# Optimization experiments

Hardware: AMD Instinct MI355X
Metric: run time of the kernel (lower is better)

The kernel has to match this reference:

```python
import jax, jax.numpy as jnp
import numpy as np

B, IN, OUT, K = 2048, 1024, 1024, 20


def setup_inputs() -> dict:
    key = jax.random.key(0)
    k1, k2 = jax.random.split(key)
    x = jax.random.normal(k1, (B, IN), dtype=jnp.float32)
    # per-output, per-input spline coefficients: (out_features, in_features, num_knots)
    W = jax.random.normal(k2, (OUT, IN, K), dtype=jnp.float32) * 0.1
    # evenly spaced knot grid on [-2, 2] (linspace)
    knots = jnp.linspace(-2.0, 2.0, K, dtype=jnp.float32)
    return {"x": x, "W": W, "knots": knots}


def reference(x, W, knots):
    # RBF spline basis shared across all output features (this is the fusion
    # the original per-output Python loop misses):
    # basis[b, i, k] = exp(-0.5 * ((x[b, i] - knots[k]) / h)^2)
    h = knots[1] - knots[0]  # uniform knot spacing -> RBF bandwidth
    basis = jnp.exp(-0.5 * jnp.square((x[:, :, None] - knots) / h))  # (B, IN, K)
    # Each SplineLayer o computes sum_{i,k} W[o,i,k] * basis[b,i,k]; the
    # KANBlock concatenates the OUT scalars -> a single einsum.
    return jnp.einsum("bik,oik->bo", basis, W)  # (B, OUT)
```

## Files before the change

### kernel.cpp

```cpp
#include <hip/hip_runtime.h>

#define B_DIM 2048
#define IN_DIM 1024
#define OUT_DIM 1024
#define K_KNOTS 20
#define KR (IN_DIM * K_KNOTS)
#define OUT_ELEMS (B_DIM * OUT_DIM)
#define KS 8

#define NPAIRS (B_DIM * IN_DIM * 5 / 2)
#define NB_BASIS_BLK (NPAIRS / 256)
#define NW4 (OUT_DIM * KR / 8)
#define NB_W_BLK (NW4 / 256)

typedef __bf16 bf16x8 __attribute__((ext_vector_type(8)));
typedef float  f32x4  __attribute__((ext_vector_type(4)));

#define MFMA16(a, b, c) __builtin_amdgcn_mfma_f32_16x16x32_bf16(a, b, c, 0, 0, 0)

__device__ __forceinline__ unsigned short f2bf(float f) {
    unsigned int u = __float_as_uint(f);
    unsigned int r = u + 0x7fffu + ((u >> 16) & 1u);
    return (unsigned short)(r >> 16);
}

__device__ __forceinline__ unsigned int pack2(float lo, float hi) {
    return (unsigned int)f2bf(lo) | ((unsigned int)f2bf(hi) << 16);
}

__device__ __forceinline__ void async_load16(const void* g, void* l) {
    __builtin_amdgcn_global_load_lds(
        (const __attribute__((address_space(1))) void*)g,
        (__attribute__((address_space(3))) void*)l,
        16, 0, 0);
}

__global__ void __launch_bounds__(256) prep_kernel(
        const float* __restrict__ x,
        const float4* __restrict__ Wsrc,
        const float* __restrict__ knots,
        uint4* __restrict__ basis_out,
        uint4* __restrict__ w_out) {
    if (blockIdx.x < NB_BASIS_BLK) {
        const unsigned int p  = blockIdx.x * 256 + threadIdx.x;
        const unsigned int n0 = 2 * p;
        const unsigned int q0  = n0 % 5u;
        const unsigned int bi0 = n0 / 5u;
        const float t0   = knots[0];
        const float h    = knots[1] - t0;
        const float invh = 1.0f / h;

        const bool cross = (q0 == 4u);
        const unsigned int bi1 = bi0 + (cross ? 1u : 0u);
        const float xv0 = x[bi0];
        const float xv1 = x[bi1];
        const float kA = (float)(4u * q0);
        const float kB = cross ? 0.f : kA + 4.f;

        float v[8];
#pragma unroll
        for (int j = 0; j < 4; ++j) {
            float t = __builtin_fmaf(kA + (float)j, h, t0);
            float d = (xv0 - t) * invh;
            v[j] = __expf(-0.5f * d * d);
        }
#pragma unroll
        for (int j = 0; j < 4; ++j) {
            float t = __builtin_fmaf(kB + (float)j, h, t0);
            float d = (xv1 - t) * invh;
            v[4 + j] = __expf(-0.5f * d * d);
        }
        uint4 o;
        o.x = pack2(v[0], v[1]); o.y = pack2(v[2], v[3]);
        o.z = pack2(v[4], v[5]); o.w = pack2(v[6], v[7]);
        basis_out[p] = o;
    } else {
        unsigned int t = (blockIdx.x - NB_BASIS_BLK) * 256 + threadIdx.x;
        float4 a = Wsrc[2 * t];
        float4 b = Wsrc[2 * t + 1];
        uint4 o;
        o.x = pack2(a.x, a.y);
        o.y = pack2(a.z, a.w);
        o.z = pack2(b.x, b.y);
        o.w = pack2(b.z, b.w);
        w_out[t] = o;
    }
}

#define AOF(s, kh) (((s) * 2 + (kh)) * 8192)
#define BOF(s, kh) (32768 + ((s) * 2 + (kh)) * 8192)

template <int S>
__device__ __forceinline__ void tile_step(
        int t, int ntiles,
        const unsigned short* __restrict__ Ab,
        const unsigned short* __restrict__ Bb,
        unsigned short* lds,
        f32x4 (&acc)[8][4],
        int m0, int n0, int k0,
        int wave, int rowA, int rowB,
        int srow32, int scol32) {
    const int kb1 = k0 + (t + 1) * 64;
    const bool st = (t + 1 < ntiles);

    auto stage_half = [&](const unsigned short* __restrict__ src, int grow,
                          int kc, int lbase) {
        const unsigned short* g =
            src + (size_t)(grow + wave * 32 + srow32) * KR + kc + scol32;
        async_load16(g,                   &lds[lbase + wave * 1024]);
        async_load16(g + (size_t)16 * KR, &lds[lbase + wave * 1024 + 512]);
    };

    bf16x8 a0[4], a1[4], b0[4], b1[4], s0[4], s1[4];

#pragma unroll
    for (int i = 0; i < 4; ++i) a0[i] = *(const bf16x8*)&lds[AOF(S, 0) + rowA + i * 512];
#pragma unroll
    for (int j = 0; j < 4; ++j) b0[j] = *(const bf16x8*)&lds[BOF(S, 0) + rowB + j * 512];
    if (st) {
        stage_half(Ab, m0, kb1, AOF(S ^ 1, 0));
        asm volatile("s_waitcnt vmcnt(2)" ::: "memory");
    } else {
        asm volatile("s_waitcnt vmcnt(0)" ::: "memory");
    }
    __builtin_amdgcn_s_barrier();
    asm volatile("s_waitcnt lgkmcnt(0)" ::: "memory");
    __builtin_amdgcn_sched_barrier(0);
    __builtin_amdgcn_s_setprio(1);
#pragma unroll
    for (int i = 0; i < 4; ++i)
#pragma unroll
        for (int j = 0; j < 4; ++j)
            acc[i][j] = MFMA16(a0[i], b0[j], acc[i][j]);
    __builtin_amdgcn_s_setprio(0);

#pragma unroll
    for (int i = 0; i < 4; ++i) a1[i] = *(const bf16x8*)&lds[AOF(S, 1) + rowA + i * 512];
#pragma unroll
    for (int j = 0; j < 4; ++j) b1[j] = *(const bf16x8*)&lds[BOF(S, 1) + rowB + j * 512];
    if (st) stage_half(Bb, n0, kb1, BOF(S ^ 1, 0));
    __builtin_amdgcn_s_barrier();
    asm volatile("s_waitcnt lgkmcnt(0)" ::: "memory");
    __builtin_amdgcn_sched_barrier(0);
    __builtin_amdgcn_s_setprio(1);
#pragma unroll
    for (int i = 0; i < 4; ++i)
#pragma unroll
        for (int j = 0; j < 4; ++j)
            acc[i][j] = MFMA16(a1[i], b1[j], acc[i][j]);
    __builtin_amdgcn_s_setprio(0);

#pragma unroll
    for (int i = 0; i < 4; ++i) s0[i] = *(const bf16x8*)&lds[AOF(S, 0) + rowA + (4 + i) * 512];
    if (st) stage_half(Ab, m0, kb1 + 32, AOF(S ^ 1, 1));
    __builtin_amdgcn_s_barrier();
    asm volatile("s_waitcnt lgkmcnt(0)" ::: "memory");
    __builtin_amdgcn_sched_barrier(0);
    __builtin_amdgcn_s_setprio(1);
#pragma unroll
    for (int i = 0; i < 4; ++i)
#pragma unroll
        for (int j = 0; j < 4; ++j)
            acc[4 + i][j] = MFMA16(s0[i], b0[j], acc[4 + i][j]);
    __builtin_amdgcn_s_setprio(0);

#pragma unroll
    for (int i = 0; i < 4; ++i) s1[i] = *(const bf16x8*)&lds[AOF(S, 1) + rowA + (4 + i) * 512];
    if (st) {
        stage_half(Bb, n0, kb1 + 32, BOF(S ^ 1, 1));
        asm volatile("s_waitcnt vmcnt(4)" ::: "memory");
    }
    __builtin_amdgcn_s_barrier();
    asm volatile("s_waitcnt lgkmcnt(0)" ::: "memory");
    __builtin_amdgcn_sched_barrier(0);
    __builtin_amdgcn_s_setprio(1);
#pragma unroll
    for (int i = 0; i < 4; ++i)
#pragma unroll
        for (int j = 0; j < 4; ++j)
            acc[4 + i][j] = MFMA16(s1[i], b1[j], acc[4 + i][j]);
    __builtin_amdgcn_s_setprio(0);
}

__global__ void __launch_bounds__(512, 2)
kan_gemm8(const unsigned short* __restrict__ Ab,
          const unsigned short* __restrict__ Bb,
          float* __restrict__ part) {
    __shared__ __align__(16) unsigned short lds[65536];

    constexpr int KPBk   = KR / KS;
    constexpr int NTILES = KPBk / 64;

    const int id  = blockIdx.x;
    const int z   = id & 7;
    const int ord = id >> 3;
    const int mt  = ord & 7;
    const int nt  = ord >> 3;
    const int m0  = mt * 256;
    const int n0  = nt * 256;
    const int k0  = z * KPBk;

    const int tid  = threadIdx.x;
    const int wave = tid >> 6;
    const int lane = tid & 63;
    const int wm   = wave >> 2;
    const int wn   = wave & 3;

    const int srow32 = lane >> 2;
    const int scol32 = ((lane & 3) ^ ((lane >> 3) & 3)) * 8;

    auto stage_half = [&](const unsigned short* __restrict__ src, int grow,
                          int kc, int lbase) {
        const unsigned short* g =
            src + (size_t)(grow + wave * 32 + srow32) * KR + kc + scol32;
        async_load16(g,                   &lds[lbase + wave * 1024]);
        async_load16(g + (size_t)16 * KR, &lds[lbase + wave * 1024 + 512]);
    };

    f32x4 acc[8][4];
#pragma unroll
    for (int i = 0; i < 8; ++i)
#pragma unroll
        for (int j = 0; j < 4; ++j) acc[i][j] = (f32x4){0.f, 0.f, 0.f, 0.f};

    const int q    = lane >> 4;
    const int r15  = lane & 15;
    const int cs   = (q ^ ((r15 >> 1) & 3)) * 8;
    const int rowA = (wm * 128 + r15) * 32 + cs;
    const int rowB = (wn * 64 + r15) * 32 + cs;

    stage_half(Ab, m0, k0,      AOF(0, 0));
    stage_half(Bb, n0, k0,      BOF(0, 0));
    stage_half(Ab, m0, k0 + 32, AOF(0, 1));
    stage_half(Bb, n0, k0 + 32, BOF(0, 1));
    asm volatile("s_waitcnt vmcnt(4)" ::: "memory");
    __builtin_amdgcn_s_barrier();

    for (int tt = 0; tt < NTILES; tt += 2) {
        tile_step<0>(tt,     NTILES, Ab, Bb, lds, acc, m0, n0, k0,
                     wave, rowA, rowB, srow32, scol32);
        tile_step<1>(tt + 1, NTILES, Ab, Bb, lds, acc, m0, n0, k0,
                     wave, rowA, rowB, srow32, scol32);
    }

    float* dst = part + (size_t)z * OUT_ELEMS;
#pragma unroll
    for (int i = 0; i < 8; ++i)
#pragma unroll
        for (int j = 0; j < 4; ++j)
#pragma unroll
            for (int r = 0; r < 4; ++r) {
                const int row = m0 + wm * 128 + i * 16 + q * 4 + r;
                const int c   = n0 + wn * 64  + j * 16 + r15;
                dst[(size_t)row * OUT_DIM + c] = acc[i][j][r];
            }
}

template <int KSr>
__global__ void kan_reduce(const float* __restrict__ part, float* __restrict__ out) {
    const int idx = (blockIdx.x * 256 + threadIdx.x) * 4;
    f32x4 s = *(const f32x4*)(part + idx);
#pragma unroll
    for (int z = 1; z < KSr; ++z)
        s += *(const f32x4*)(part + (size_t)z * OUT_ELEMS + idx);
    *(f32x4*)(out + idx) = s;
}

__global__ void kan_fallback(const float* __restrict__ x,
                             const float* __restrict__ W,
                             const float* __restrict__ knots,
                             float* __restrict__ out) {
    __shared__ float basis[256 * K_KNOTS];
    const int b = blockIdx.x;
    const int o = blockIdx.y * blockDim.x + threadIdx.x;
    const float invh = 1.0f / (knots[1] - knots[0]);
    const float* w = W + (size_t)o * KR;
    float sum = 0.f;
    for (int i0 = 0; i0 < IN_DIM; i0 += 256) {
        __syncthreads();
        for (int idx = threadIdx.x; idx < 256 * K_KNOTS; idx += blockDim.x) {
            const int i = i0 + idx / K_KNOTS;
            const int k = idx % K_KNOTS;
            const float d = (x[(size_t)b * IN_DIM + i] - knots[k]) * invh;
            basis[idx] = __expf(-0.5f * d * d);
        }
        __syncthreads();
        for (int r = 0; r < 256 * K_KNOTS; ++r)
            sum += basis[r] * w[(size_t)i0 * K_KNOTS + r];
    }
    out[(size_t)b * OUT_DIM + o] = sum;
}

extern "C" void kernel_launch(void* const* d_in, const int* in_sizes, int n_in,
                              void* d_out, int out_size, void* d_ws, size_t ws_size,
                              hipStream_t stream) {
    const float* x     = (const float*)d_in[0];
    const float* W     = (const float*)d_in[1];
    const float* knots = (const float*)d_in[2];
    float* out = (float*)d_out;

    const size_t basis_bytes = (size_t)B_DIM * KR * 2;
    const size_t wb_bytes    = (size_t)OUT_DIM * KR * 2;
    const size_t part_bytes  = (size_t)KS * OUT_ELEMS * 4;

    unsigned short* Ab = (unsigned short*)d_ws;
    unsigned short* Bb = (unsigned short*)((char*)d_ws + basis_bytes);
    float* part = (float*)((char*)d_ws + basis_bytes + wb_bytes);

    if (ws_size >= basis_bytes + wb_bytes + part_bytes) {
        prep_kernel<<<dim3(NB_BASIS_BLK + NB_W_BLK), dim3(256), 0, stream>>>(
            x, (const float4*)W, knots, (uint4*)Ab, (uint4*)Bb);
        kan_gemm8<<<dim3(256), dim3(512), 0, stream>>>(Ab, Bb, part);
        kan_reduce<KS><<<dim3(OUT_ELEMS / (256 * 4)), dim3(256), 0, stream>>>(part, out);
    } else {
        kan_fallback<<<dim3(B_DIM, OUT_DIM / 256), dim3(256), 0, stream>>>(x, W, knots, out);
    }
}
```

Baseline: 244.9 us.

## Prefetch next MFMA phase LDS fragments before current phase compute

Software-pipelines the LDS-to-register fragment loads in the GEMM tile step. Each phase now issues the reads for the next phase before running its MFMAs, and waits only with a partial lgkmcnt. The a0/b0 fragments of the next tile are loaded at the end of the previous tile and carried across calls. This aims to hide LDS read latency behind matrix-core work, at the cost of more live VGPRs and tighter reliance on the barrier ordering staying correct.

```diff
diff --git a/kernel.cpp b/kernel.cpp
--- a/kernel.cpp
+++ b/kernel.cpp
@@ -97,6 +97,7 @@
         const unsigned short* __restrict__ Bb,
         unsigned short* lds,
         f32x4 (&acc)[8][4],
+        bf16x8 (&a0)[4], bf16x8 (&b0)[4],
         int m0, int n0, int k0,
         int wave, int rowA, int rowB,
         int srow32, int scol32) {
@@ -111,12 +112,8 @@
         async_load16(g + (size_t)16 * KR, &lds[lbase + wave * 1024 + 512]);
     };
 
-    bf16x8 a0[4], a1[4], b0[4], b1[4], s0[4], s1[4];
-
-#pragma unroll
-    for (int i = 0; i < 4; ++i) a0[i] = *(const bf16x8*)&lds[AOF(S, 0) + rowA + i * 512];
-#pragma unroll
-    for (int j = 0; j < 4; ++j) b0[j] = *(const bf16x8*)&lds[BOF(S, 0) + rowB + j * 512];
+    bf16x8 a1[4], b1[4], s0[4], s1[4];
+
     if (st) {
         stage_half(Ab, m0, kb1, AOF(S ^ 1, 0));
         asm volatile("s_waitcnt vmcnt(2)" ::: "memory");
@@ -124,7 +121,13 @@
         asm volatile("s_waitcnt vmcnt(0)" ::: "memory");
     }
     __builtin_amdgcn_s_barrier();
-    asm volatile("s_waitcnt lgkmcnt(0)" ::: "memory");
+    asm volatile("" ::: "memory");
+#pragma unroll
+    for (int i = 0; i < 4; ++i) a1[i] = *(const bf16x8*)&lds[AOF(S, 1) + rowA + i * 512];
+#pragma unroll
+    for (int j = 0; j < 4; ++j) b1[j] = *(const bf16x8*)&lds[BOF(S, 1) + rowB + j * 512];
+    __builtin_amdgcn_sched_barrier(0);
+    asm volatile("s_waitcnt lgkmcnt(8)" ::: "memory");
     __builtin_amdgcn_sched_barrier(0);
     __builtin_amdgcn_s_setprio(1);
 #pragma unroll
@@ -134,13 +137,13 @@
             acc[i][j] = MFMA16(a0[i], b0[j], acc[i][j]);
     __builtin_amdgcn_s_setprio(0);
 
-#pragma unroll
-    for (int i = 0; i < 4; ++i) a1[i] = *(const bf16x8*)&lds[AOF(S, 1) + rowA + i * 512];
-#pragma unroll
-    for (int j = 0; j < 4; ++j) b1[j] = *(const bf16x8*)&lds[BOF(S, 1) + rowB + j * 512];
     if (st) stage_half(Bb, n0, kb1, BOF(S ^ 1, 0));
     __builtin_amdgcn_s_barrier();
-    asm volatile("s_waitcnt lgkmcnt(0)" ::: "memory");
+    asm volatile("" ::: "memory");
+#pragma unroll
+    for (int i = 0; i < 4; ++i) s0[i] = *(const bf16x8*)&lds[AOF(S, 0) + rowA + (4 + i) * 512];
+    __builtin_amdgcn_sched_barrier(0);
+    asm volatile("s_waitcnt lgkmcnt(4)" ::: "memory");
     __builtin_amdgcn_sched_barrier(0);
     __builtin_amdgcn_s_setprio(1);
 #pragma unroll
@@ -150,11 +153,13 @@
             acc[i][j] = MFMA16(a1[i], b1[j], acc[i][j]);
     __builtin_amdgcn_s_setprio(0);
 
-#pragma unroll
-    for (int i = 0; i < 4; ++i) s0[i] = *(const bf16x8*)&lds[AOF(S, 0) + rowA + (4 + i) * 512];
     if (st) stage_half(Ab, m0, kb1 + 32, AOF(S ^ 1, 1));
     __builtin_amdgcn_s_barrier();
-    asm volatile("s_waitcnt lgkmcnt(0)" ::: "memory");
+    asm volatile("" ::: "memory");
+#pragma unroll
+    for (int i = 0; i < 4; ++i) s1[i] = *(const bf16x8*)&lds[AOF(S, 1) + rowA + (4 + i) * 512];
+    __builtin_amdgcn_sched_barrier(0);
+    asm volatile("s_waitcnt lgkmcnt(4)" ::: "memory");
     __builtin_amdgcn_sched_barrier(0);
     __builtin_amdgcn_s_setprio(1);
 #pragma unroll
@@ -164,14 +169,22 @@
             acc[4 + i][j] = MFMA16(s0[i], b0[j], acc[4 + i][j]);
     __builtin_amdgcn_s_setprio(0);
 
-#pragma unroll
-    for (int i = 0; i < 4; ++i) s1[i] = *(const bf16x8*)&lds[AOF(S, 1) + rowA + (4 + i) * 512];
     if (st) {
         stage_half(Bb, n0, kb1 + 32, BOF(S ^ 1, 1));
         asm volatile("s_waitcnt vmcnt(4)" ::: "memory");
     }
     __builtin_amdgcn_s_barrier();
-    asm volatile("s_waitcnt lgkmcnt(0)" ::: "memory");
+    asm volatile("" ::: "memory");
+    if (st) {
+#pragma unroll
+        for (int i = 0; i < 4; ++i) a0[i] = *(const bf16x8*)&lds[AOF(S ^ 1, 0) + rowA + i * 512];
+#pragma unroll
+        for (int j = 0; j < 4; ++j) b0[j] = *(const bf16x8*)&lds[BOF(S ^ 1, 0) + rowB + j * 512];
+        __builtin_amdgcn_sched_barrier(0);
+        asm volatile("s_waitcnt lgkmcnt(8)" ::: "memory");
+    } else {
+        asm volatile("s_waitcnt lgkmcnt(0)" ::: "memory");
+    }
     __builtin_amdgcn_sched_barrier(0);
     __builtin_amdgcn_s_setprio(1);
 #pragma unroll
@@ -235,11 +248,18 @@
     stage_half(Bb, n0, k0 + 32, BOF(0, 1));
     asm volatile("s_waitcnt vmcnt(4)" ::: "memory");
     __builtin_amdgcn_s_barrier();
+    asm volatile("" ::: "memory");
+    bf16x8 a0[4], b0[4];
+#pragma unroll
+    for (int i = 0; i < 4; ++i) a0[i] = *(const bf16x8*)&lds[AOF(0, 0) + rowA + i * 512];
+#pragma unroll
+    for (int j = 0; j < 4; ++j) b0[j] = *(const bf16x8*)&lds[BOF(0, 0) + rowB + j * 512];
+    __builtin_amdgcn_sched_barrier(0);
 
     for (int tt = 0; tt < NTILES; tt += 2) {
-        tile_step<0>(tt,     NTILES, Ab, Bb, lds, acc, m0, n0, k0,
+        tile_step<0>(tt,     NTILES, Ab, Bb, lds, acc, a0, b0, m0, n0, k0,
                      wave, rowA, rowB, srow32, scol32);
-        tile_step<1>(tt + 1, NTILES, Ab, Bb, lds, acc, m0, n0, k0,
+        tile_step<1>(tt + 1, NTILES, Ab, Bb, lds, acc, a0, b0, m0, n0, k0,
                      wave, rowA, rowB, srow32, scol32);
     }
 
```

After: 259.9 us. +6.1%, slower.
